# Performance work log

Hardware: AMD Instinct MI355X
Metric: run time of the kernel (lower is better)

Reference implementation:

```python
import jax, jax.numpy as jnp
import numpy as np

BATCH = 256
SEQ = 2048        # sequences (in_features of each per-channel Linear)
C = 32            # input_size (number of independent channels/layers)
EMB = 2048        # embedding_dim (out_features)


def setup_inputs() -> dict:
    key = jax.random.key(0)
    kx, kw, kb = jax.random.split(key, 3)
    x = jax.random.normal(kx, (BATCH, SEQ, C), dtype=jnp.float32)
    # PyTorch nn.Linear init: U(-1/sqrt(fan_in), 1/sqrt(fan_in))
    bound = 1.0 / np.sqrt(SEQ)
    W = jax.random.uniform(kw, (C, SEQ, EMB), minval=-bound, maxval=bound, dtype=jnp.float32)
    b = jax.random.uniform(kb, (C, EMB), minval=-bound, maxval=bound, dtype=jnp.float32)
    return {"x": x, "W": W, "b": b}


def reference(x, W, b):
    # x: (B, S, C) -> transpose to (B, C, S); per-channel Linear + ReLU.
    # Grouped GEMM: out[b,c,e] = relu(sum_s x[b,s,c] * W[c,s,e] + b[c,e])
    xc = jnp.transpose(x, (0, 2, 1))                 # (B, C, S)
    out = jnp.einsum('bcs,cse->bce', xc, W) + b      # (B, C, E)
    return jax.nn.relu(out)
```

## Files before the change

kernel.cpp:

```cpp
#include <hip/hip_runtime.h>

#define BATCH 256
#define SEQ   2048
#define NC    32
#define EMB   2048
#define NT    32

typedef unsigned short ushort_t;
using f32x4  = __attribute__((ext_vector_type(4))) float;
using bf16x8 = __attribute__((ext_vector_type(8))) short;

using u32_gl = __attribute__((address_space(1))) const unsigned int;
using u32_ld = __attribute__((address_space(3))) unsigned int;

__device__ __forceinline__ unsigned short f2bf(float f) {
  unsigned int u = __float_as_uint(f);
  u += 0x7FFFu + ((u >> 16) & 1u);
  return (unsigned short)(u >> 16);
}

__global__ __launch_bounds__(256) void transpose_x_kernel(
    const float* __restrict__ x, ushort_t* __restrict__ xT) {
  __shared__ float tile[64][33];
  const int b  = blockIdx.x >> 5;
  const int st = blockIdx.x & 31;
  const int t  = threadIdx.x;
  const float* src = x + ((size_t)b * SEQ + (size_t)st * 64) * NC;
#pragma unroll
  for (int i = 0; i < 2; ++i) {
    int idx = t + i * 256;
    float4 v = reinterpret_cast<const float4*>(src)[idx];
    int s = idx >> 3;
    int c = (idx & 7) * 4;
    tile[s][c + 0] = v.x; tile[s][c + 1] = v.y;
    tile[s][c + 2] = v.z; tile[s][c + 3] = v.w;
  }
  __syncthreads();
  const int c  = t >> 3;
  const int si = (t & 7) * 8;
  unsigned int q[4];
#pragma unroll
  for (int p = 0; p < 4; ++p) {
    unsigned int h0 = f2bf(tile[si + 2 * p + 0][c]);
    unsigned int h1 = f2bf(tile[si + 2 * p + 1][c]);
    q[p] = h0 | (h1 << 16);
  }
  ushort_t* dst = xT + (size_t)c * (BATCH * SEQ) + (size_t)b * SEQ + st * 64 + si;
  *reinterpret_cast<uint4*>(dst) = make_uint4(q[0], q[1], q[2], q[3]);
}

template <int P>
__device__ __forceinline__ void gemm_iter(
    int t, const ushort_t* __restrict__ xTc, const float* __restrict__ Wc,
    char* AldsB, char* BldsB, f32x4 (&wv)[2][8], f32x4 (&acc)[4][4],
    int tid, int wr, int wc, int g, int lm, int b0, int e0) {
  const int srow8 = tid >> 5;
  const int e4    = tid & 31;

  asm volatile("s_waitcnt vmcnt(4)" ::: "memory");
#pragma unroll
  for (int i = 0; i < 4; ++i) {
    const int e_local = e4 * 4 + i;
    unsigned int q0 = (unsigned)f2bf(wv[P][0][i]) | ((unsigned)f2bf(wv[P][1][i]) << 16);
    unsigned int q1 = (unsigned)f2bf(wv[P][2][i]) | ((unsigned)f2bf(wv[P][3][i]) << 16);
    unsigned int q2 = (unsigned)f2bf(wv[P][4][i]) | ((unsigned)f2bf(wv[P][5][i]) << 16);
    unsigned int q3 = (unsigned)f2bf(wv[P][6][i]) | ((unsigned)f2bf(wv[P][7][i]) << 16);
    int byte = (e_local * 128 + srow8 * 16) ^ ((e_local & 7) << 4);
    *reinterpret_cast<uint4*>(BldsB + P * 16384 + byte) = make_uint4(q0, q1, q2, q3);
  }

  {
    const int tn = (t + 1) & (NT - 1);
    const float* wp = Wc + (size_t)(tn * 64 + srow8 * 8) * EMB + e0 + e4 * 4;
#pragma unroll
    for (int r = 0; r < 8; ++r)
      wv[P ^ 1][r] = *reinterpret_cast<const f32x4*>(wp + (size_t)r * EMB);
  }

  asm volatile("s_waitcnt lgkmcnt(0)" ::: "memory");
  __builtin_amdgcn_s_barrier();

  {
    const int s0n = ((t + 1) & (NT - 1)) * 64;
#pragma unroll
    for (int i = 0; i < 4; ++i) {
      int ch   = i * 256 + tid;
      int m    = ch >> 3;
      int slot = (ch & 7) ^ (m & 7);
      const ushort_t* src = xTc + (size_t)(b0 + m) * SEQ + s0n + slot * 8;
      __builtin_amdgcn_global_load_lds(
          (u32_gl*)src, (u32_ld*)(AldsB + (P ^ 1) * 16384 + ch * 16), 16, 0, 0);
    }
  }

  asm volatile("s_waitcnt vmcnt(12)" ::: "memory");
  __builtin_amdgcn_sched_barrier(0);

  __builtin_amdgcn_s_barrier();

#pragma unroll
  for (int ks = 0; ks < 2; ++ks) {
    bf16x8 af[4], bfr[4];
#pragma unroll
    for (int mi = 0; mi < 4; ++mi) {
      int m_local = wr * 64 + mi * 16 + lm;
      int byte = (m_local * 128 + (ks * 4 + g) * 16) ^ ((m_local & 7) << 4);
      af[mi] = *reinterpret_cast<const bf16x8*>(AldsB + P * 16384 + byte);
    }
#pragma unroll
    for (int ni = 0; ni < 4; ++ni) {
      int e_local = wc * 64 + ni * 16 + lm;
      int byte = (e_local * 128 + (ks * 4 + g) * 16) ^ ((e_local & 7) << 4);
      bfr[ni] = *reinterpret_cast<const bf16x8*>(BldsB + P * 16384 + byte);
    }
#pragma unroll
    for (int mi = 0; mi < 4; ++mi)
#pragma unroll
      for (int ni = 0; ni < 4; ++ni)
        acc[mi][ni] = __builtin_amdgcn_mfma_f32_16x16x32_bf16(
            af[mi], bfr[ni], acc[mi][ni], 0, 0, 0);
  }
}

__global__ __launch_bounds__(256, 2) void grouped_gemm_pipe(
    const ushort_t* __restrict__ xT,
    const float* __restrict__ W,
    const float* __restrict__ bias,
    float* __restrict__ out) {
  __shared__ ushort_t Alds[2][128 * 64];
  __shared__ ushort_t Blds[2][128 * 64];

  const int nwg = NC * 2 * (EMB / 128);
  const int bid = (blockIdx.x % 8) * (nwg / 8) + blockIdx.x / 8;
  const int c   = bid >> 5;
  const int et  = (bid >> 1) & 15;
  const int bt  = bid & 1;
  const int b0  = bt * 128;
  const int e0  = et * 128;

  const int tid  = threadIdx.x;
  const int w    = tid >> 6;
  const int wr   = w >> 1;
  const int wc   = w & 1;
  const int lane = tid & 63;
  const int g    = lane >> 4;
  const int lm   = lane & 15;

  const float* Wc = W + (size_t)c * SEQ * EMB;
  const ushort_t* xTc = xT + (size_t)c * (BATCH * SEQ);
  char* AldsB = (char*)&Alds[0][0];
  char* BldsB = (char*)&Blds[0][0];

  f32x4 wv[2][8];
  f32x4 acc[4][4];
#pragma unroll
  for (int i = 0; i < 4; ++i)
#pragma unroll
    for (int j = 0; j < 4; ++j) acc[i][j] = (f32x4){0.f, 0.f, 0.f, 0.f};

  {
    const int srow8 = tid >> 5;
    const int e4    = tid & 31;
    const float* wp = Wc + (size_t)(srow8 * 8) * EMB + e0 + e4 * 4;
#pragma unroll
    for (int r = 0; r < 8; ++r)
      wv[0][r] = *reinterpret_cast<const f32x4*>(wp + (size_t)r * EMB);
#pragma unroll
    for (int i = 0; i < 4; ++i) {
      int ch   = i * 256 + tid;
      int m    = ch >> 3;
      int slot = (ch & 7) ^ (m & 7);
      const ushort_t* src = xTc + (size_t)(b0 + m) * SEQ + slot * 8;
      __builtin_amdgcn_global_load_lds(
          (u32_gl*)src, (u32_ld*)(AldsB + ch * 16), 16, 0, 0);
    }
  }

  for (int t = 0; t < NT; t += 2) {
    gemm_iter<0>(t,     xTc, Wc, AldsB, BldsB, wv, acc, tid, wr, wc, g, lm, b0, e0);
    gemm_iter<1>(t + 1, xTc, Wc, AldsB, BldsB, wv, acc, tid, wr, wc, g, lm, b0, e0);
  }

  asm volatile("s_waitcnt vmcnt(0)" ::: "memory");

  const float* bc = bias + (size_t)c * EMB;
#pragma unroll
  for (int ni = 0; ni < 4; ++ni) {
    const int e = e0 + wc * 64 + ni * 16 + lm;
    const float bv = bc[e];
#pragma unroll
    for (int mi = 0; mi < 4; ++mi) {
      f32x4 a = acc[mi][ni];
      const int mbase = b0 + wr * 64 + mi * 16 + g * 4;
#pragma unroll
      for (int r = 0; r < 4; ++r) {
        float v = a[r] + bv;
        v = fmaxf(v, 0.f);
        out[((size_t)(mbase + r) * NC + c) * EMB + e] = v;
      }
    }
  }
}

__global__ __launch_bounds__(256, 2) void grouped_gemm_fallback(
    const float* __restrict__ x, const float* __restrict__ W,
    const float* __restrict__ bias, float* __restrict__ out) {
  __shared__ ushort_t Alds[128 * 64];
  __shared__ ushort_t Blds[128 * 64];
  const int bid = blockIdx.x;
  const int c   = bid >> 5;
  const int et  = (bid >> 1) & 15;
  const int bt  = bid & 1;
  const int b0  = bt * 128;
  const int e0  = et * 128;
  const int tid  = threadIdx.x;
  const int w    = tid >> 6;
  const int wr   = w >> 1;
  const int wc   = w & 1;
  const int lane = tid & 63;
  const int g    = lane >> 4;
  const int lm   = lane & 15;
  const float* Wc = W + (size_t)c * SEQ * EMB;
  const int srow8 = tid >> 5;
  const int e4    = tid & 31;
  f32x4 acc[4][4];
#pragma unroll
  for (int i = 0; i < 4; ++i)
#pragma unroll
    for (int j = 0; j < 4; ++j) acc[i][j] = (f32x4){0.f, 0.f, 0.f, 0.f};
  for (int s0 = 0; s0 < SEQ; s0 += 64) {
#pragma unroll
    for (int i = 0; i < 4; ++i) {
      int ch   = i * 256 + tid;
      int m    = ch >> 3;
      int slot = (ch & 7) ^ (m & 7);
      const float* src = x + (size_t)(b0 + m) * (SEQ * NC)
                           + (size_t)(s0 + slot * 8) * NC + c;
      unsigned int q[4];
#pragma unroll
      for (int p = 0; p < 4; ++p) {
        unsigned int h0 = f2bf(src[(2 * p + 0) * NC]);
        unsigned int h1 = f2bf(src[(2 * p + 1) * NC]);
        q[p] = h0 | (h1 << 16);
      }
      *reinterpret_cast<uint4*>((char*)&Alds[0] + ch * 16) =
          make_uint4(q[0], q[1], q[2], q[3]);
    }
    {
      const float* wp = Wc + (size_t)(s0 + srow8 * 8) * EMB + e0 + e4 * 4;
      f32x4 wvv[8];
#pragma unroll
      for (int r = 0; r < 8; ++r)
        wvv[r] = *reinterpret_cast<const f32x4*>(wp + (size_t)r * EMB);
#pragma unroll
      for (int i = 0; i < 4; ++i) {
        const int e_local = e4 * 4 + i;
        unsigned int q0 = (unsigned)f2bf(wvv[0][i]) | ((unsigned)f2bf(wvv[1][i]) << 16);
        unsigned int q1 = (unsigned)f2bf(wvv[2][i]) | ((unsigned)f2bf(wvv[3][i]) << 16);
        unsigned int q2 = (unsigned)f2bf(wvv[4][i]) | ((unsigned)f2bf(wvv[5][i]) << 16);
        unsigned int q3 = (unsigned)f2bf(wvv[6][i]) | ((unsigned)f2bf(wvv[7][i]) << 16);
        int byte = (e_local * 128 + srow8 * 16) ^ ((e_local & 7) << 4);
        *reinterpret_cast<uint4*>((char*)&Blds[0] + byte) =
            make_uint4(q0, q1, q2, q3);
      }
    }
    __syncthreads();
#pragma unroll
    for (int ks = 0; ks < 2; ++ks) {
      bf16x8 af[4], bfr[4];
#pragma unroll
      for (int mi = 0; mi < 4; ++mi) {
        int m_local = wr * 64 + mi * 16 + lm;
        int byte = (m_local * 128 + (ks * 4 + g) * 16) ^ ((m_local & 7) << 4);
        af[mi] = *reinterpret_cast<const bf16x8*>((const char*)&Alds[0] + byte);
      }
#pragma unroll
      for (int ni = 0; ni < 4; ++ni) {
        int e_local = wc * 64 + ni * 16 + lm;
        int byte = (e_local * 128 + (ks * 4 + g) * 16) ^ ((e_local & 7) << 4);
        bfr[ni] = *reinterpret_cast<const bf16x8*>((const char*)&Blds[0] + byte);
      }
#pragma unroll
      for (int mi = 0; mi < 4; ++mi)
#pragma unroll
        for (int ni = 0; ni < 4; ++ni)
          acc[mi][ni] = __builtin_amdgcn_mfma_f32_16x16x32_bf16(
              af[mi], bfr[ni], acc[mi][ni], 0, 0, 0);
    }
    __syncthreads();
  }
  const float* bc = bias + (size_t)c * EMB;
#pragma unroll
  for (int ni = 0; ni < 4; ++ni) {
    const int e = e0 + wc * 64 + ni * 16 + lm;
    const float bv = bc[e];
#pragma unroll
    for (int mi = 0; mi < 4; ++mi) {
      f32x4 a = acc[mi][ni];
      const int mbase = b0 + wr * 64 + mi * 16 + g * 4;
#pragma unroll
      for (int r = 0; r < 4; ++r) {
        float v = a[r] + bv;
        v = fmaxf(v, 0.f);
        out[((size_t)(mbase + r) * NC + c) * EMB + e] = v;
      }
    }
  }
}

extern "C" void kernel_launch(void* const* d_in, const int* in_sizes, int n_in,
                              void* d_out, int out_size, void* d_ws, size_t ws_size,
                              hipStream_t stream) {
  const float* x    = (const float*)d_in[0];
  const float* W    = (const float*)d_in[1];
  const float* bias = (const float*)d_in[2];
  float* out        = (float*)d_out;

  const size_t xT_bytes = (size_t)NC * BATCH * SEQ * sizeof(ushort_t);

  if (ws_size >= xT_bytes) {
    ushort_t* xT = (ushort_t*)d_ws;
    transpose_x_kernel<<<BATCH * (SEQ / 64), 256, 0, stream>>>(x, xT);
    grouped_gemm_pipe<<<NC * 2 * (EMB / 128), 256, 0, stream>>>(xT, W, bias, out);
  } else {
    grouped_gemm_fallback<<<NC * 2 * (EMB / 128), 256, 0, stream>>>(x, W, bias, out);
  }
}
```

Baseline: 182.2 us.

## Use 512-thread blocks covering full batch so each W tile is converted once

Each workgroup grows to 512 threads (8 waves) and covers all 256 batch rows for one channel and 128-column output tile, instead of two 128-row blocks per tile. Each W slice is loaded and converted from fp32 to bf16 only once rather than twice, halving global W traffic and conversion work. The per-thread W load shrinks to 4 rows, the A LDS buffer doubles to 256 rows, and the grid halves to 512 blocks. The cost is more LDS per block and fewer blocks, which may reduce occupancy or leave CUs idle.

```diff
diff --git a/kernel.cpp b/kernel.cpp
--- a/kernel.cpp
+++ b/kernel.cpp
@@ -52,9 +52,9 @@
 template <int P>
 __device__ __forceinline__ void gemm_iter(
     int t, const ushort_t* __restrict__ xTc, const float* __restrict__ Wc,
-    char* AldsB, char* BldsB, f32x4 (&wv)[2][8], f32x4 (&acc)[4][4],
-    int tid, int wr, int wc, int g, int lm, int b0, int e0) {
-  const int srow8 = tid >> 5;
+    char* AldsB, char* BldsB, f32x4 (&wv)[2][4], f32x4 (&acc)[4][4],
+    int tid, int wr, int wc, int g, int lm, int e0) {
+  const int srow4 = tid >> 5;
   const int e4    = tid & 31;
 
   asm volatile("s_waitcnt vmcnt(4)" ::: "memory");
@@ -63,17 +63,15 @@
     const int e_local = e4 * 4 + i;
     unsigned int q0 = (unsigned)f2bf(wv[P][0][i]) | ((unsigned)f2bf(wv[P][1][i]) << 16);
     unsigned int q1 = (unsigned)f2bf(wv[P][2][i]) | ((unsigned)f2bf(wv[P][3][i]) << 16);
-    unsigned int q2 = (unsigned)f2bf(wv[P][4][i]) | ((unsigned)f2bf(wv[P][5][i]) << 16);
-    unsigned int q3 = (unsigned)f2bf(wv[P][6][i]) | ((unsigned)f2bf(wv[P][7][i]) << 16);
-    int byte = (e_local * 128 + srow8 * 16) ^ ((e_local & 7) << 4);
-    *reinterpret_cast<uint4*>(BldsB + P * 16384 + byte) = make_uint4(q0, q1, q2, q3);
+    int byte = (e_local * 128 + srow4 * 8) ^ ((e_local & 7) << 4);
+    *reinterpret_cast<uint2*>(BldsB + P * 16384 + byte) = make_uint2(q0, q1);
   }
 
   {
     const int tn = (t + 1) & (NT - 1);
-    const float* wp = Wc + (size_t)(tn * 64 + srow8 * 8) * EMB + e0 + e4 * 4;
-#pragma unroll
-    for (int r = 0; r < 8; ++r)
+    const float* wp = Wc + (size_t)(tn * 64 + srow4 * 4) * EMB + e0 + e4 * 4;
+#pragma unroll
+    for (int r = 0; r < 4; ++r)
       wv[P ^ 1][r] = *reinterpret_cast<const f32x4*>(wp + (size_t)r * EMB);
   }
 
@@ -84,16 +82,16 @@
     const int s0n = ((t + 1) & (NT - 1)) * 64;
 #pragma unroll
     for (int i = 0; i < 4; ++i) {
-      int ch   = i * 256 + tid;
+      int ch   = i * 512 + tid;
       int m    = ch >> 3;
       int slot = (ch & 7) ^ (m & 7);
-      const ushort_t* src = xTc + (size_t)(b0 + m) * SEQ + s0n + slot * 8;
+      const ushort_t* src = xTc + (size_t)m * SEQ + s0n + slot * 8;
       __builtin_amdgcn_global_load_lds(
-          (u32_gl*)src, (u32_ld*)(AldsB + (P ^ 1) * 16384 + ch * 16), 16, 0, 0);
-    }
-  }
-
-  asm volatile("s_waitcnt vmcnt(12)" ::: "memory");
+          (u32_gl*)src, (u32_ld*)(AldsB + (P ^ 1) * 32768 + ch * 16), 16, 0, 0);
+    }
+  }
+
+  asm volatile("s_waitcnt vmcnt(8)" ::: "memory");
   __builtin_amdgcn_sched_barrier(0);
 
   __builtin_amdgcn_s_barrier();
@@ -105,7 +103,7 @@
     for (int mi = 0; mi < 4; ++mi) {
       int m_local = wr * 64 + mi * 16 + lm;
       int byte = (m_local * 128 + (ks * 4 + g) * 16) ^ ((m_local & 7) << 4);
-      af[mi] = *reinterpret_cast<const bf16x8*>(AldsB + P * 16384 + byte);
+      af[mi] = *reinterpret_cast<const bf16x8*>(AldsB + P * 32768 + byte);
     }
 #pragma unroll
     for (int ni = 0; ni < 4; ++ni) {
@@ -122,20 +120,17 @@
   }
 }
 
-__global__ __launch_bounds__(256, 2) void grouped_gemm_pipe(
+__global__ __launch_bounds__(512, 2) void grouped_gemm_pipe(
     const ushort_t* __restrict__ xT,
     const float* __restrict__ W,
     const float* __restrict__ bias,
     float* __restrict__ out) {
-  __shared__ ushort_t Alds[2][128 * 64];
+  __shared__ ushort_t Alds[2][256 * 64];
   __shared__ ushort_t Blds[2][128 * 64];
 
-  const int nwg = NC * 2 * (EMB / 128);
-  const int bid = (blockIdx.x % 8) * (nwg / 8) + blockIdx.x / 8;
-  const int c   = bid >> 5;
-  const int et  = (bid >> 1) & 15;
-  const int bt  = bid & 1;
-  const int b0  = bt * 128;
+  const int bid = (blockIdx.x & 7) * 64 + (blockIdx.x >> 3);
+  const int c   = bid >> 4;
+  const int et  = bid & 15;
   const int e0  = et * 128;
 
   const int tid  = threadIdx.x;
@@ -151,7 +146,7 @@
   char* AldsB = (char*)&Alds[0][0];
   char* BldsB = (char*)&Blds[0][0];
 
-  f32x4 wv[2][8];
+  f32x4 wv[2][4];
   f32x4 acc[4][4];
 #pragma unroll
   for (int i = 0; i < 4; ++i)
@@ -159,26 +154,26 @@
     for (int j = 0; j < 4; ++j) acc[i][j] = (f32x4){0.f, 0.f, 0.f, 0.f};
 
   {
-    const int srow8 = tid >> 5;
+    const int srow4 = tid >> 5;
     const int e4    = tid & 31;
-    const float* wp = Wc + (size_t)(srow8 * 8) * EMB + e0 + e4 * 4;
-#pragma unroll
-    for (int r = 0; r < 8; ++r)
+    const float* wp = Wc + (size_t)(srow4 * 4) * EMB + e0 + e4 * 4;
+#pragma unroll
+    for (int r = 0; r < 4; ++r)
       wv[0][r] = *reinterpret_cast<const f32x4*>(wp + (size_t)r * EMB);
 #pragma unroll
     for (int i = 0; i < 4; ++i) {
-      int ch   = i * 256 + tid;
+      int ch   = i * 512 + tid;
       int m    = ch >> 3;
       int slot = (ch & 7) ^ (m & 7);
-      const ushort_t* src = xTc + (size_t)(b0 + m) * SEQ + slot * 8;
+      const ushort_t* src = xTc + (size_t)m * SEQ + slot * 8;
       __builtin_amdgcn_global_load_lds(
           (u32_gl*)src, (u32_ld*)(AldsB + ch * 16), 16, 0, 0);
     }
   }
 
   for (int t = 0; t < NT; t += 2) {
-    gemm_iter<0>(t,     xTc, Wc, AldsB, BldsB, wv, acc, tid, wr, wc, g, lm, b0, e0);
-    gemm_iter<1>(t + 1, xTc, Wc, AldsB, BldsB, wv, acc, tid, wr, wc, g, lm, b0, e0);
+    gemm_iter<0>(t,     xTc, Wc, AldsB, BldsB, wv, acc, tid, wr, wc, g, lm, e0);
+    gemm_iter<1>(t + 1, xTc, Wc, AldsB, BldsB, wv, acc, tid, wr, wc, g, lm, e0);
   }
 
   asm volatile("s_waitcnt vmcnt(0)" ::: "memory");
@@ -191,7 +186,7 @@
 #pragma unroll
     for (int mi = 0; mi < 4; ++mi) {
       f32x4 a = acc[mi][ni];
-      const int mbase = b0 + wr * 64 + mi * 16 + g * 4;
+      const int mbase = wr * 64 + mi * 16 + g * 4;
 #pragma unroll
       for (int r = 0; r < 4; ++r) {
         float v = a[r] + bv;
@@ -321,7 +316,7 @@
   if (ws_size >= xT_bytes) {
     ushort_t* xT = (ushort_t*)d_ws;
     transpose_x_kernel<<<BATCH * (SEQ / 64), 256, 0, stream>>>(x, xT);
-    grouped_gemm_pipe<<<NC * 2 * (EMB / 128), 256, 0, stream>>>(xT, W, bias, out);
+    grouped_gemm_pipe<<<NC * (EMB / 128), 512, 0, stream>>>(xT, W, bias, out);
   } else {
     grouped_gemm_fallback<<<NC * 2 * (EMB / 128), 256, 0, stream>>>(x, W, bias, out);
   }
```

Result: faster. 158.5 us (-13.0%).
